# Kernel optimization log

Measured on AMD Instinct MI355X. Metric: run time of the kernel, lower is better.

The kernel has to match this reference:

```python
import jax, jax.numpy as jnp
import numpy as np

B, T, N = 16, 1024, 512        # batch, time tokens, neurons
DK_T, DK_S = 64, 128           # key dims (temporal, spatial)
# dim_T = N, dim_S = T, dim_value_T = N (required by cross einsum), heads = 1


def setup_inputs() -> dict:
    key = jax.random.key(0)
    ks = jax.random.split(key, 11)
    return {
        "x_T": jax.random.normal(ks[0], (B, T, N), jnp.float32),
        "x_S": jax.random.normal(ks[1], (B, N, T), jnp.float32),
        "Wq_T": jax.random.normal(ks[2], (N, DK_T), jnp.float32) * 0.05,
        "Wk_T": jax.random.normal(ks[3], (N, DK_T), jnp.float32) * 0.05,
        "Wv_T": jax.random.normal(ks[4], (N, N), jnp.float32) * 0.05,
        "Wq_S": jax.random.normal(ks[5], (T, DK_S), jnp.float32) * 0.05,
        "Wk_S": jax.random.normal(ks[6], (T, DK_S), jnp.float32) * 0.05,
        "Wout_T": jax.random.normal(ks[7], (N, N), jnp.float32) * 0.05,
        "bout_T": jax.random.normal(ks[8], (N,), jnp.float32) * 0.05,
        "bias_T": jax.random.normal(ks[9], (1, 1, 1, DK_T), jnp.float32),
        "bias_S": jax.random.normal(ks[10], (1, 1, 1, DK_S), jnp.float32),
    }


def reference(x_T, x_S, Wq_T, Wk_T, Wv_T, Wq_S, Wk_S, Wout_T, bout_T, bias_T, bias_S):
    scale_T = DK_T ** -0.5
    scale_S = DK_S ** -0.5
    # Temporal attention: tokens along time axis, heads=1 -> add h axis
    q_T = (x_T @ Wq_T)[:, None] * scale_T          # [b,1,t,dk_T]
    k_T = (x_T @ Wk_T)[:, None]                    # [b,1,t,dk_T]
    v_T = (x_T @ Wv_T)[:, None]                    # [b,1,t,n]  (dim_value_T = n)
    logits_T = jnp.einsum('bhid,bhjd->bhij', q_T + bias_T, k_T)  # [b,1,t,t]
    attn_T = jax.nn.softmax(logits_T, axis=-1)
    out_T = jnp.einsum('bhij,bhjd->bhid', attn_T, v_T)            # [b,1,t,n]
    # Spatial attention: tokens along neuron axis
    q_S = (x_S @ Wq_S)[:, None] * scale_S          # [b,1,n,dk_S]
    k_S = (x_S @ Wk_S)[:, None]                    # [b,1,n,dk_S]
    logits_S = jnp.einsum('bhid,bhjd->bhij', q_S + bias_S, k_S)   # [b,1,n,n]
    attn_S = jax.nn.softmax(logits_S, axis=-1)
    # spatial_temporal_1 cross combination: attn_S mixes the neuron axis of out_T
    out_T = jnp.einsum('bhij,bhtj->bhti', attn_S, out_T)          # [b,1,t,n]
    out_T = out_T.reshape(B, T, N)                 # 'b h t d -> b t (h d)'
    out_T = out_T @ Wout_T + bout_T                # to_out_T
    return jnp.transpose(out_T, (0, 2, 1))         # [b, n, t]
```

## Files before the change

### kernel.cpp

```cpp
#include <hip/hip_runtime.h>
#include <cstddef>

typedef short short8 __attribute__((ext_vector_type(8)));
typedef unsigned short ushortx8 __attribute__((ext_vector_type(8)));
typedef float floatx4 __attribute__((ext_vector_type(4)));

__device__ __forceinline__ unsigned int bf16_rne(float x) {
    unsigned int u = __float_as_uint(x);
    return (u + 0x7fffu + ((u >> 16) & 1u)) >> 16;
}

__device__ __forceinline__ void split4(const floatx4 v,
                                       unsigned long long& hp,
                                       unsigned long long& lp) {
    unsigned int h[4], l[4];
    #pragma unroll
    for (int j = 0; j < 4; ++j) {
        h[j] = bf16_rne(v[j]);
        float hf = __uint_as_float(h[j] << 16);
        l[j] = bf16_rne(v[j] - hf);
    }
    hp = (unsigned long long)(h[0] | (h[1] << 16)) |
         ((unsigned long long)(h[2] | (h[3] << 16)) << 32);
    lp = (unsigned long long)(l[0] | (l[1] << 16)) |
         ((unsigned long long)(l[2] | (l[3] << 16)) << 32);
}

__device__ __forceinline__ unsigned long long pack_hi4(const floatx4 v) {
    unsigned int h0 = bf16_rne(v[0]), h1 = bf16_rne(v[1]);
    unsigned int h2 = bf16_rne(v[2]), h3 = bf16_rne(v[3]);
    return (unsigned long long)(h0 | (h1 << 16)) |
           ((unsigned long long)(h2 | (h3 << 16)) << 32);
}

template<int BM, int BN, int AMODE, int BMODE, int OUTMODE, bool HASBIAS>
__global__ __launch_bounds__(256, 2)
void gemm_nt(const void* __restrict__ Ah_, const void* __restrict__ Al_,
             const void* __restrict__ Bh_, const void* __restrict__ Bl_,
             void* __restrict__ C_, void* __restrict__ Cl_,
             const float* __restrict__ bias,
             int K, int lda, int ldb, int ldc,
             long sA, long sB, long sC, float alpha, int nsplit)
{
    constexpr bool ALO = (AMODE == 1 || AMODE == 3);
    constexpr bool BLO = (BMODE == 1 || BMODE == 3);
    constexpr int LS = 40;
    __shared__ unsigned short Ash[2][BM][LS];
    __shared__ unsigned short Als[2][ALO ? BM : 1][LS];
    __shared__ unsigned short Bsh[2][BN][LS];
    __shared__ unsigned short Bls[2][BLO ? BN : 1][LS];

    const unsigned int gx = gridDim.x;
    const unsigned int nwg = gx * gridDim.y;
    unsigned int flat = blockIdx.y * gx + blockIdx.x;
    {
        unsigned int qq = nwg >> 3, rr = nwg & 7;
        unsigned int xcd = flat & 7, idx = flat >> 3;
        flat = (xcd < rr) ? (xcd * (qq + 1) + idx)
                          : (rr * (qq + 1) + (xcd - rr) * qq + idx);
    }
    const int b   = blockIdx.z;
    const int bm0 = (flat / gx) * BM;
    const int bn0 = (flat % gx) * BN;
    const int tid  = threadIdx.x;
    const int lane = tid & 63;
    const int wid  = tid >> 6;
    const int wr = wid >> 1, wc = wid & 1;
    constexpr int WM = BM / 2, WN = BN / 2;
    constexpr int FM = WM / 16, FN = WN / 16;
    floatx4 acc[FM][FN] = {};
    const int l15  = lane & 15;
    const int koff = (lane >> 4) * 8;

    constexpr int ACHF = BM * 32 / 4, NAF0 = (ACHF + 255) / 256;
    constexpr int ACHH = BM * 32 / 8, NAH0 = (ACHH + 255) / 256;
    constexpr int BCHF = BN * 32 / 4, NBF0 = (BCHF + 255) / 256;
    constexpr int BCHH = BN * 32 / 8, NBH0 = (BCHH + 255) / 256;
    constexpr int NAF = (AMODE <= 1) ? NAF0 : 1;
    constexpr int NAH = (AMODE >= 2) ? NAH0 : 1;
    constexpr int NBF = (BMODE <= 1) ? NBF0 : 1;
    constexpr int NBH = (BMODE >= 2) ? NBH0 : 1;
    floatx4  aF[NAF], bF[NBF];
    ushortx8 aH[NAH], aL[NAH], bH[NBH], bL[NBH];

    auto loadA = [&](int k0) {
        if (AMODE <= 1) {
            const float* A = (const float*)Ah_ + (long)b * sA;
            #pragma unroll
            for (int i = 0; i < NAF; ++i) {
                int idx = i * 256 + tid;
                if (ACHF % 256 == 0 || idx < ACHF) {
                    int flatc = idx * 4;
                    int r = flatc >> 5, c = flatc & 31;
                    aF[i] = *(const floatx4*)(A + (long)(bm0 + r) * lda + k0 + c);
                }
            }
        } else {
            const unsigned short* A  = (const unsigned short*)Ah_ + (long)b * sA;
            const unsigned short* Al = (const unsigned short*)Al_ + (long)b * sA;
            #pragma unroll
            for (int i = 0; i < NAH; ++i) {
                int idx = i * 256 + tid;
                if (ACHH % 256 == 0 || idx < ACHH) {
                    int flatc = idx * 8;
                    int r = flatc >> 5, c = flatc & 31;
                    aH[i] = *(const ushortx8*)(A + (long)(bm0 + r) * lda + k0 + c);
                    if (AMODE == 3)
                        aL[i] = *(const ushortx8*)(Al + (long)(bm0 + r) * lda + k0 + c);
                }
            }
        }
    };
    auto loadB = [&](int k0) {
        if (BMODE <= 1) {
            const float* Bp = (const float*)Bh_ + (long)b * sB;
            #pragma unroll
            for (int i = 0; i < NBF; ++i) {
                int idx = i * 256 + tid;
                if (BCHF % 256 == 0 || idx < BCHF) {
                    int flatc = idx * 4;
                    int r = flatc >> 5, c = flatc & 31;
                    bF[i] = *(const floatx4*)(Bp + (long)(bn0 + r) * ldb + k0 + c);
                }
            }
        } else {
            const unsigned short* Bp = (const unsigned short*)Bh_ + (long)b * sB;
            const unsigned short* Bl = (const unsigned short*)Bl_ + (long)b * sB;
            #pragma unroll
            for (int i = 0; i < NBH; ++i) {
                int idx = i * 256 + tid;
                if (BCHH % 256 == 0 || idx < BCHH) {
                    int flatc = idx * 8;
                    int r = flatc >> 5, c = flatc & 31;
                    bH[i] = *(const ushortx8*)(Bp + (long)(bn0 + r) * ldb + k0 + c);
                    if (BMODE == 3)
                        bL[i] = *(const ushortx8*)(Bl + (long)(bn0 + r) * ldb + k0 + c);
                }
            }
        }
    };
    auto writeA = [&](int bf) {
        if (AMODE <= 1) {
            #pragma unroll
            for (int i = 0; i < NAF; ++i) {
                int idx = i * 256 + tid;
                if (ACHF % 256 == 0 || idx < ACHF) {
                    int flatc = idx * 4;
                    int r = flatc >> 5, c = flatc & 31;
                    if (AMODE == 1) {
                        unsigned long long hp, lp; split4(aF[i], hp, lp);
                        *(unsigned long long*)&Ash[bf][r][c] = hp;
                        *(unsigned long long*)&Als[bf][r][c] = lp;
                    } else {
                        *(unsigned long long*)&Ash[bf][r][c] = pack_hi4(aF[i]);
                    }
                }
            }
        } else {
            #pragma unroll
            for (int i = 0; i < NAH; ++i) {
                int idx = i * 256 + tid;
                if (ACHH % 256 == 0 || idx < ACHH) {
                    int flatc = idx * 8;
                    int r = flatc >> 5, c = flatc & 31;
                    *(ushortx8*)&Ash[bf][r][c] = aH[i];
                    if (AMODE == 3) *(ushortx8*)&Als[bf][r][c] = aL[i];
                }
            }
        }
    };
    auto writeB = [&](int bf) {
        if (BMODE <= 1) {
            #pragma unroll
            for (int i = 0; i < NBF; ++i) {
                int idx = i * 256 + tid;
                if (BCHF % 256 == 0 || idx < BCHF) {
                    int flatc = idx * 4;
                    int r = flatc >> 5, c = flatc & 31;
                    if (BMODE == 1) {
                        unsigned long long hp, lp; split4(bF[i], hp, lp);
                        *(unsigned long long*)&Bsh[bf][r][c] = hp;
                        *(unsigned long long*)&Bls[bf][r][c] = lp;
                    } else {
                        *(unsigned long long*)&Bsh[bf][r][c] = pack_hi4(bF[i]);
                    }
                }
            }
        } else {
            #pragma unroll
            for (int i = 0; i < NBH; ++i) {
                int idx = i * 256 + tid;
                if (BCHH % 256 == 0 || idx < BCHH) {
                    int flatc = idx * 8;
                    int r = flatc >> 5, c = flatc & 31;
                    *(ushortx8*)&Bsh[bf][r][c] = bH[i];
                    if (BMODE == 3) *(ushortx8*)&Bls[bf][r][c] = bL[i];
                }
            }
        }
    };
    auto compute = [&](int bf) {
        short8 ah[FM], al[FM], bh[FN], bl[FN];
        #pragma unroll
        for (int mi = 0; mi < FM; ++mi) {
            ah[mi] = *(const short8*)&Ash[bf][wr * WM + mi * 16 + l15][koff];
            if (ALO) al[mi] = *(const short8*)&Als[bf][wr * WM + mi * 16 + l15][koff];
        }
        #pragma unroll
        for (int ni = 0; ni < FN; ++ni) {
            bh[ni] = *(const short8*)&Bsh[bf][wc * WN + ni * 16 + l15][koff];
            if (BLO) bl[ni] = *(const short8*)&Bls[bf][wc * WN + ni * 16 + l15][koff];
        }
        #pragma unroll
        for (int mi = 0; mi < FM; ++mi)
            #pragma unroll
            for (int ni = 0; ni < FN; ++ni) {
                if (ALO)
                    acc[mi][ni] = __builtin_amdgcn_mfma_f32_16x16x32_bf16(
                        al[mi], bh[ni], acc[mi][ni], 0, 0, 0);
                if (BLO)
                    acc[mi][ni] = __builtin_amdgcn_mfma_f32_16x16x32_bf16(
                        ah[mi], bl[ni], acc[mi][ni], 0, 0, 0);
                acc[mi][ni] = __builtin_amdgcn_mfma_f32_16x16x32_bf16(
                    ah[mi], bh[ni], acc[mi][ni], 0, 0, 0);
            }
    };

    loadA(0); loadB(0);
    writeA(0); writeB(0);
    __syncthreads();
    int cur = 0;
    for (int k0 = 32; k0 < K; k0 += 32) {
        loadA(k0); loadB(k0);
        compute(cur);
        writeA(cur ^ 1); writeB(cur ^ 1);
        __syncthreads();
        cur ^= 1;
    }
    compute(cur);

    const int rq = (lane >> 4) * 4;
    #pragma unroll
    for (int mi = 0; mi < FM; ++mi) {
        #pragma unroll
        for (int ni = 0; ni < FN; ++ni) {
            int gm = bm0 + wr * WM + mi * 16 + rq;
            int gn = bn0 + wc * WN + ni * 16 + l15;
            float ae = (gn < nsplit) ? alpha : 1.0f;
            float be = 0.f;
            if (HASBIAS) be = (gn < nsplit) ? bias[gn] : 0.0f;
            float vals[4];
            #pragma unroll
            for (int j = 0; j < 4; ++j) vals[j] = acc[mi][ni][j] * ae + be;
            if (OUTMODE == 0) {
                float* C = (float*)C_ + (long)b * sC;
                #pragma unroll
                for (int j = 0; j < 4; ++j) C[(long)(gm + j) * ldc + gn] = vals[j];
            } else if (OUTMODE == 1) {
                float* C = (float*)C_ + (long)b * sC;
                floatx4 o;
                #pragma unroll
                for (int j = 0; j < 4; ++j) o[j] = vals[j];
                *(floatx4*)(C + (long)gn * ldc + gm) = o;
            } else if (OUTMODE == 2) {
                unsigned short* Ch = (unsigned short*)C_ + (long)b * sC;
                unsigned short* Cl = (unsigned short*)Cl_ + (long)b * sC;
                #pragma unroll
                for (int j = 0; j < 4; ++j) {
                    unsigned int h = bf16_rne(vals[j]);
                    float hf = __uint_as_float(h << 16);
                    unsigned int lo = bf16_rne(vals[j] - hf);
                    Ch[(long)(gm + j) * ldc + gn] = (unsigned short)h;
                    Cl[(long)(gm + j) * ldc + gn] = (unsigned short)lo;
                }
            } else {
                unsigned short* Ch = (unsigned short*)C_ + (long)b * sC;
                #pragma unroll
                for (int j = 0; j < 4; ++j)
                    Ch[(long)(gm + j) * ldc + gn] = (unsigned short)bf16_rne(vals[j]);
            }
        }
    }
}

template<int COLS, int DK, int LDQK>
__global__ __launch_bounds__(256, 2)
void qk_softmax(const unsigned short* __restrict__ qk_h,
                const unsigned short* __restrict__ qk_l,
                unsigned short* __restrict__ P)
{
    constexpr int WCOLS = COLS / 4;
    constexpr int FN = WCOLS / 16;
    constexpr int QPAD = DK + 24;
    __shared__ unsigned short Qh[32][QPAD];
    __shared__ unsigned short Ql[32][QPAD];
    __shared__ float red[32][4];
    __shared__ unsigned short Pl[32][COLS + 8];

    const int b  = blockIdx.y;
    const int q0 = blockIdx.x * 32;
    const long rowBase = (long)b * COLS;
    const int tid = threadIdx.x;
    const int lane = tid & 63, wid = tid >> 6;
    const int l15 = lane & 15, g = lane >> 4;
    const int koff = g * 8;

    constexpr int QCH = DK / 8;
    for (int i = tid; i < 32 * QCH; i += 256) {
        int r = i / QCH, c = (i % QCH) * 8;
        *(ushortx8*)&Qh[r][c] = *(const ushortx8*)(qk_h + (rowBase + q0 + r) * LDQK + c);
        *(ushortx8*)&Ql[r][c] = *(const ushortx8*)(qk_l + (rowBase + q0 + r) * LDQK + c);
    }
    __syncthreads();

    floatx4 acc[2][FN] = {};
    const unsigned short* kh = qk_h + rowBase * LDQK + DK;
    const unsigned short* kl = qk_l + rowBase * LDQK + DK;

    #pragma unroll
    for (int kk = 0; kk < DK; kk += 32) {
        short8 ah[2], al[2];
        #pragma unroll
        for (int mi = 0; mi < 2; ++mi) {
            ah[mi] = *(const short8*)&Qh[mi * 16 + l15][kk + koff];
            al[mi] = *(const short8*)&Ql[mi * 16 + l15][kk + koff];
        }
        #pragma unroll
        for (int ni = 0; ni < FN; ++ni) {
            long krow = wid * WCOLS + ni * 16 + l15;
            short8 bh = *(const short8*)(kh + krow * LDQK + kk + koff);
            short8 bl = *(const short8*)(kl + krow * LDQK + kk + koff);
            #pragma unroll
            for (int mi = 0; mi < 2; ++mi) {
                acc[mi][ni] = __builtin_amdgcn_mfma_f32_16x16x32_bf16(al[mi], bh, acc[mi][ni], 0, 0, 0);
                acc[mi][ni] = __builtin_amdgcn_mfma_f32_16x16x32_bf16(ah[mi], bl, acc[mi][ni], 0, 0, 0);
                acc[mi][ni] = __builtin_amdgcn_mfma_f32_16x16x32_bf16(ah[mi], bh, acc[mi][ni], 0, 0, 0);
            }
        }
    }

    float pm[2][4];
    #pragma unroll
    for (int mi = 0; mi < 2; ++mi)
        #pragma unroll
        for (int j = 0; j < 4; ++j) {
            float m = acc[mi][0][j];
            #pragma unroll
            for (int ni = 1; ni < FN; ++ni) m = fmaxf(m, acc[mi][ni][j]);
            pm[mi][j] = m;
        }
    #pragma unroll
    for (int msk = 1; msk < 16; msk <<= 1) {
        #pragma unroll
        for (int mi = 0; mi < 2; ++mi)
            #pragma unroll
            for (int j = 0; j < 4; ++j)
                pm[mi][j] = fmaxf(pm[mi][j], __shfl_xor(pm[mi][j], msk));
    }
    if (l15 == 0) {
        #pragma unroll
        for (int mi = 0; mi < 2; ++mi)
            #pragma unroll
            for (int j = 0; j < 4; ++j) red[mi * 16 + g * 4 + j][wid] = pm[mi][j];
    }
    __syncthreads();
    float rm[2][4];
    #pragma unroll
    for (int mi = 0; mi < 2; ++mi)
        #pragma unroll
        for (int j = 0; j < 4; ++j) {
            const float* r4 = red[mi * 16 + g * 4 + j];
            rm[mi][j] = fmaxf(fmaxf(r4[0], r4[1]), fmaxf(r4[2], r4[3]));
        }
    __syncthreads();

    float ps[2][4] = {};
    #pragma unroll
    for (int mi = 0; mi < 2; ++mi)
        #pragma unroll
        for (int ni = 0; ni < FN; ++ni)
            #pragma unroll
            for (int j = 0; j < 4; ++j) {
                float e = __expf(acc[mi][ni][j] - rm[mi][j]);
                acc[mi][ni][j] = e;
                ps[mi][j] += e;
            }
    #pragma unroll
    for (int msk = 1; msk < 16; msk <<= 1) {
        #pragma unroll
        for (int mi = 0; mi < 2; ++mi)
            #pragma unroll
            for (int j = 0; j < 4; ++j)
                ps[mi][j] += __shfl_xor(ps[mi][j], msk);
    }
    if (l15 == 0) {
        #pragma unroll
        for (int mi = 0; mi < 2; ++mi)
            #pragma unroll
            for (int j = 0; j < 4; ++j) red[mi * 16 + g * 4 + j][wid] = ps[mi][j];
    }
    __syncthreads();
    float inv[2][4];
    #pragma unroll
    for (int mi = 0; mi < 2; ++mi)
        #pragma unroll
        for (int j = 0; j < 4; ++j) {
            const float* r4 = red[mi * 16 + g * 4 + j];
            inv[mi][j] = 1.0f / (r4[0] + r4[1] + r4[2] + r4[3]);
        }

    #pragma unroll
    for (int mi = 0; mi < 2; ++mi)
        #pragma unroll
        for (int ni = 0; ni < FN; ++ni)
            #pragma unroll
            for (int j = 0; j < 4; ++j)
                Pl[mi * 16 + g * 4 + j][wid * WCOLS + ni * 16 + l15] =
                    (unsigned short)bf16_rne(acc[mi][ni][j] * inv[mi][j]);
    __syncthreads();

    constexpr int PCH = COLS / 8;
    for (int i = tid; i < 32 * PCH; i += 256) {
        int r = i / PCH, c = (i % PCH) * 8;
        *(ushortx8*)(P + (rowBase + q0 + r) * COLS + c) = *(const ushortx8*)&Pl[r][c];
    }
}

__global__ __launch_bounds__(256)
void transpose_split(const float* __restrict__ in,
                     unsigned short* __restrict__ outH,
                     unsigned short* __restrict__ outL,
                     int R, int C, int rowOff, int ldo)
{
    __shared__ float tile[32][33];
    const int tc = blockIdx.x * 32, tr = blockIdx.y * 32;
    const int x = threadIdx.x, y = threadIdx.y;
    #pragma unroll
    for (int i = 0; i < 32; i += 8)
        tile[y + i][x] = in[(long)(tr + y + i) * C + tc + x];
    __syncthreads();
    #pragma unroll
    for (int i = 0; i < 32; i += 8) {
        float v = tile[x][y + i];
        unsigned int h = bf16_rne(v);
        float hf = __uint_as_float(h << 16);
        unsigned int lo = bf16_rne(v - hf);
        long idx = (long)(tc + y + i + rowOff) * ldo + tr + x;
        outH[idx] = (unsigned short)h;
        outL[idx] = (unsigned short)lo;
    }
}

extern "C" void kernel_launch(void* const* d_in, const int* in_sizes, int n_in,
                              void* d_out, int out_size, void* d_ws, size_t ws_size,
                              hipStream_t stream)
{
    (void)in_sizes; (void)n_in; (void)out_size; (void)ws_size;
    const float* x_T    = (const float*)d_in[0];
    const float* x_S    = (const float*)d_in[1];
    const float* Wq_T   = (const float*)d_in[2];
    const float* Wk_T   = (const float*)d_in[3];
    const float* Wv_T   = (const float*)d_in[4];
    const float* Wq_S   = (const float*)d_in[5];
    const float* Wk_S   = (const float*)d_in[6];
    const float* Wout_T = (const float*)d_in[7];
    const float* bout_T = (const float*)d_in[8];
    const float* bias_T = (const float*)d_in[9];
    const float* bias_S = (const float*)d_in[10];
    float* out = (float*)d_out;

    constexpr int B = 16, T = 1024, N = 512, DKT = 64, DKS = 128;
    typedef unsigned short us;

    char* w = (char*)d_ws;
    size_t off = 0;
    auto alloc = [&](size_t bytes) { char* p = w + off; off = (off + bytes + 255) & ~(size_t)255; return p; };
    us* wqkT_h = (us*)alloc(128 * 512 * 2);
    us* wqkT_l = (us*)alloc(128 * 512 * 2);
    us* wvt_h  = (us*)alloc(512 * 512 * 2);
    us* wvt_l  = (us*)alloc(512 * 512 * 2);
    us* wqks_h = (us*)alloc(256 * 1024 * 2);
    us* wqks_l = (us*)alloc(256 * 1024 * 2);
    us* wout_h = (us*)alloc(512 * 512 * 2);
    us* wout_l = (us*)alloc(512 * 512 * 2);
    us* qk_h   = (us*)alloc((size_t)16384 * 128 * 2);
    us* qk_l   = (us*)alloc((size_t)16384 * 128 * 2);
    us* P_T    = (us*)alloc((size_t)B * T * T * 2);
    us* P_S    = (us*)alloc((size_t)B * N * N * 2);
    us* vT_h   = (us*)alloc((size_t)B * N * T * 2);
    us* vT_l   = (us*)alloc((size_t)B * N * T * 2);
    us* outT_h = (us*)alloc((size_t)B * T * N * 2);
    us* outT_l = (us*)alloc((size_t)B * T * N * 2);
    us* out2_h = vT_h;
    us* out2_l = vT_l;

    const float scale_T = 0.125f;
    const float scale_S = 0.088388347648318447f;
    const int BIG = 1 << 30;

    dim3 tb(32, 8);
    transpose_split<<<dim3(2, 16),  tb, 0, stream>>>(Wq_T,   wqkT_h, wqkT_l, 512, 64,   0, 512);
    transpose_split<<<dim3(2, 16),  tb, 0, stream>>>(Wk_T,   wqkT_h, wqkT_l, 512, 64,  64, 512);
    transpose_split<<<dim3(16, 16), tb, 0, stream>>>(Wv_T,   wvt_h,  wvt_l,  512, 512,  0, 512);
    transpose_split<<<dim3(4, 32),  tb, 0, stream>>>(Wq_S,   wqks_h, wqks_l, 1024, 128, 0, 1024);
    transpose_split<<<dim3(4, 32),  tb, 0, stream>>>(Wk_S,   wqks_h, wqks_l, 1024, 128, 128, 1024);
    transpose_split<<<dim3(16, 16), tb, 0, stream>>>(Wout_T, wout_h, wout_l, 512, 512,  0, 512);

    gemm_nt<32, 128, 1, 3, 2, true><<<dim3(1, 512, 1), 256, 0, stream>>>(
        x_T, nullptr, wqkT_h, wqkT_l, qk_h, qk_l, bias_T,
        512, 512, 512, 128, 0, 0, 0, scale_T, 64);
    gemm_nt<128, 128, 3, 0, 3, false><<<dim3(8, 4, B), 256, 0, stream>>>(
        wvt_h, wvt_l, x_T, nullptr, vT_h, nullptr, nullptr,
        512, 512, 512, 1024, 0, (long)T * N, (long)N * T, 1.0f, 0);
    qk_softmax<1024, 64, 128><<<dim3(32, 16), 256, 0, stream>>>(qk_h, qk_l, P_T);
    gemm_nt<128, 128, 2, 2, 2, false><<<dim3(4, 8, B), 256, 0, stream>>>(
        P_T, nullptr, vT_h, nullptr, outT_h, outT_l, nullptr,
        1024, 1024, 1024, 512, (long)T * T, (long)N * T, (long)T * N, 1.0f, 0);

    gemm_nt<32, 128, 1, 3, 2, true><<<dim3(2, 256, 1), 256, 0, stream>>>(
        x_S, nullptr, wqks_h, wqks_l, qk_h, qk_l, bias_S,
        1024, 1024, 1024, 256, 0, 0, 0, scale_S, 128);
    qk_softmax<512, 128, 256><<<dim3(16, 16), 256, 0, stream>>>(qk_h, qk_l, P_S);
    gemm_nt<128, 128, 3, 2, 2, false><<<dim3(4, 8, B), 256, 0, stream>>>(
        outT_h, outT_l, P_S, nullptr, out2_h, out2_l, nullptr,
        512, 512, 512, 512, (long)T * N, (long)N * N, (long)T * N, 1.0f, 0);
    gemm_nt<128, 128, 3, 2, 1, true><<<dim3(4, 8, B), 256, 0, stream>>>(
        out2_h, out2_l, wout_h, nullptr, out, nullptr, bout_T,
        512, 512, 512, 1024, (long)T * N, 0, (long)N * T, 1.0f, BIG);
}
```

Before: 221.8 us.

## Split-K the Q/K projection GEMMs with a separate reduce-and-split kernel

Replaces the two Q/K projection GEMMs (x_T and x_S against stacked Wq/Wk) with a dedicated 4-way split-K kernel that writes fp32 partials into the P_T scratch buffer. A reduce kernel then sums the partials, applies scale and bias to the query half, and splits the result into bf16 hi/lo. This raises the block count for these narrow-N projections to improve CU occupancy. In exchange it adds an extra launch and fp32 partial traffic through global memory. It also drops the B-lo product term, which the original mode 2 also lacked.

After: 224.9 us. Within noise of the previous version (+1.4%).

```diff
diff --git a/kernel.cpp b/kernel.cpp
--- a/kernel.cpp
+++ b/kernel.cpp
@@ -3,6 +3,7 @@
 
 typedef short short8 __attribute__((ext_vector_type(8)));
 typedef unsigned short ushortx8 __attribute__((ext_vector_type(8)));
+typedef unsigned short ushortx4 __attribute__((ext_vector_type(4)));
 typedef float floatx4 __attribute__((ext_vector_type(4)));
 
 __device__ __forceinline__ unsigned int bf16_rne(float x) {
@@ -90,8 +91,7 @@
             for (int i = 0; i < NAF; ++i) {
                 int idx = i * 256 + tid;
                 if (ACHF % 256 == 0 || idx < ACHF) {
-                    int flatc = idx * 4;
-                    int r = flatc >> 5, c = flatc & 31;
+                    int fc = idx * 4; int r = fc >> 5, c = fc & 31;
                     aF[i] = *(const floatx4*)(A + (long)(bm0 + r) * lda + k0 + c);
                 }
             }
@@ -102,8 +102,7 @@
             for (int i = 0; i < NAH; ++i) {
                 int idx = i * 256 + tid;
                 if (ACHH % 256 == 0 || idx < ACHH) {
-                    int flatc = idx * 8;
-                    int r = flatc >> 5, c = flatc & 31;
+                    int fc = idx * 8; int r = fc >> 5, c = fc & 31;
                     aH[i] = *(const ushortx8*)(A + (long)(bm0 + r) * lda + k0 + c);
                     if (AMODE == 3)
                         aL[i] = *(const ushortx8*)(Al + (long)(bm0 + r) * lda + k0 + c);
@@ -118,8 +117,7 @@
             for (int i = 0; i < NBF; ++i) {
                 int idx = i * 256 + tid;
                 if (BCHF % 256 == 0 || idx < BCHF) {
-                    int flatc = idx * 4;
-                    int r = flatc >> 5, c = flatc & 31;
+                    int fc = idx * 4; int r = fc >> 5, c = fc & 31;
                     bF[i] = *(const floatx4*)(Bp + (long)(bn0 + r) * ldb + k0 + c);
                 }
             }
@@ -130,8 +128,7 @@
             for (int i = 0; i < NBH; ++i) {
                 int idx = i * 256 + tid;
                 if (BCHH % 256 == 0 || idx < BCHH) {
-                    int flatc = idx * 8;
-                    int r = flatc >> 5, c = flatc & 31;
+                    int fc = idx * 8; int r = fc >> 5, c = fc & 31;
                     bH[i] = *(const ushortx8*)(Bp + (long)(bn0 + r) * ldb + k0 + c);
                     if (BMODE == 3)
                         bL[i] = *(const ushortx8*)(Bl + (long)(bn0 + r) * ldb + k0 + c);
@@ -145,8 +142,7 @@
             for (int i = 0; i < NAF; ++i) {
                 int idx = i * 256 + tid;
                 if (ACHF % 256 == 0 || idx < ACHF) {
-                    int flatc = idx * 4;
-                    int r = flatc >> 5, c = flatc & 31;
+                    int fc = idx * 4; int r = fc >> 5, c = fc & 31;
                     if (AMODE == 1) {
                         unsigned long long hp, lp; split4(aF[i], hp, lp);
                         *(unsigned long long*)&Ash[bf][r][c] = hp;
@@ -161,8 +157,7 @@
             for (int i = 0; i < NAH; ++i) {
                 int idx = i * 256 + tid;
                 if (ACHH % 256 == 0 || idx < ACHH) {
-                    int flatc = idx * 8;
-                    int r = flatc >> 5, c = flatc & 31;
+                    int fc = idx * 8; int r = fc >> 5, c = fc & 31;
                     *(ushortx8*)&Ash[bf][r][c] = aH[i];
                     if (AMODE == 3) *(ushortx8*)&Als[bf][r][c] = aL[i];
                 }
@@ -175,8 +170,7 @@
             for (int i = 0; i < NBF; ++i) {
                 int idx = i * 256 + tid;
                 if (BCHF % 256 == 0 || idx < BCHF) {
-                    int flatc = idx * 4;
-                    int r = flatc >> 5, c = flatc & 31;
+                    int fc = idx * 4; int r = fc >> 5, c = fc & 31;
                     if (BMODE == 1) {
                         unsigned long long hp, lp; split4(bF[i], hp, lp);
                         *(unsigned long long*)&Bsh[bf][r][c] = hp;
@@ -191,8 +185,7 @@
             for (int i = 0; i < NBH; ++i) {
                 int idx = i * 256 + tid;
                 if (BCHH % 256 == 0 || idx < BCHH) {
-                    int flatc = idx * 8;
-                    int r = flatc >> 5, c = flatc & 31;
+                    int fc = idx * 8; int r = fc >> 5, c = fc & 31;
                     *(ushortx8*)&Bsh[bf][r][c] = bH[i];
                     if (BMODE == 3) *(ushortx8*)&Bls[bf][r][c] = bL[i];
                 }
@@ -283,6 +276,114 @@
     }
 }
 
+template<int KCH>
+__global__ __launch_bounds__(256, 6)
+void proj_splitk(const float* __restrict__ A, const unsigned short* __restrict__ Bp,
+                 float* __restrict__ Cpart, int lda, int ldb, int ldc, long MN)
+{
+    __shared__ unsigned short Ah[32][40];
+    __shared__ unsigned short Al[32][40];
+    __shared__ unsigned short Bs[128][40];
+
+    const int tid = threadIdx.x;
+    const int lane = tid & 63, wid = tid >> 6;
+    const int wr = wid >> 1, wc = wid & 1;
+    const int l15 = lane & 15, g = lane >> 4;
+    const int koff = g * 8;
+    const int bm0 = blockIdx.y * 32;
+    const int bn0 = blockIdx.x * 128;
+    const int kbase = blockIdx.z * KCH;
+
+    const int ar = tid >> 3, ac = (tid & 7) * 4;
+    floatx4 aReg;
+    ushortx8 bReg[2];
+
+    auto load = [&](int k0) {
+        aReg = *(const floatx4*)(A + (long)(bm0 + ar) * lda + k0 + ac);
+        #pragma unroll
+        for (int i = 0; i < 2; ++i) {
+            int fc = (i * 256 + tid) * 8;
+            int r = fc >> 5, c = fc & 31;
+            bReg[i] = *(const ushortx8*)(Bp + (long)(bn0 + r) * ldb + k0 + c);
+        }
+    };
+    auto store_lds = [&]() {
+        unsigned long long hp, lp; split4(aReg, hp, lp);
+        *(unsigned long long*)&Ah[ar][ac] = hp;
+        *(unsigned long long*)&Al[ar][ac] = lp;
+        #pragma unroll
+        for (int i = 0; i < 2; ++i) {
+            int fc = (i * 256 + tid) * 8;
+            int r = fc >> 5, c = fc & 31;
+            *(ushortx8*)&Bs[r][c] = bReg[i];
+        }
+    };
+
+    floatx4 acc[4] = {};
+    auto compute = [&]() {
+        short8 ah = *(const short8*)&Ah[wr * 16 + l15][koff];
+        short8 al = *(const short8*)&Al[wr * 16 + l15][koff];
+        #pragma unroll
+        for (int ni = 0; ni < 4; ++ni) {
+            short8 bh = *(const short8*)&Bs[wc * 64 + ni * 16 + l15][koff];
+            acc[ni] = __builtin_amdgcn_mfma_f32_16x16x32_bf16(al, bh, acc[ni], 0, 0, 0);
+            acc[ni] = __builtin_amdgcn_mfma_f32_16x16x32_bf16(ah, bh, acc[ni], 0, 0, 0);
+        }
+    };
+
+    load(kbase);
+    store_lds();
+    __syncthreads();
+    #pragma unroll 1
+    for (int s = 1; s < KCH / 32; ++s) {
+        load(kbase + s * 32);
+        compute();
+        __syncthreads();
+        store_lds();
+        __syncthreads();
+    }
+    compute();
+
+    float* C = Cpart + (long)blockIdx.z * MN;
+    #pragma unroll
+    for (int ni = 0; ni < 4; ++ni) {
+        int gn = bn0 + wc * 64 + ni * 16 + l15;
+        #pragma unroll
+        for (int j = 0; j < 4; ++j)
+            C[(long)(bm0 + wr * 16 + g * 4 + j) * ldc + gn] = acc[ni][j];
+    }
+}
+
+__global__ __launch_bounds__(256)
+void reduce_split(const float* __restrict__ Cp, long MN, int colMask, int nsplit,
+                  float alpha, const float* __restrict__ bias,
+                  unsigned short* __restrict__ H, unsigned short* __restrict__ L)
+{
+    long n4 = MN >> 2;
+    for (long i = (long)blockIdx.x * 256 + threadIdx.x; i < n4;
+         i += (long)gridDim.x * 256) {
+        long e = i << 2;
+        floatx4 v = *(const floatx4*)(Cp + e);
+        v += *(const floatx4*)(Cp + MN + e);
+        v += *(const floatx4*)(Cp + 2 * MN + e);
+        v += *(const floatx4*)(Cp + 3 * MN + e);
+        int colb = (int)(e & colMask);
+        ushortx4 h4, l4;
+        #pragma unroll
+        for (int j = 0; j < 4; ++j) {
+            float x = v[j];
+            int col = colb + j;
+            if (col < nsplit) x = x * alpha + bias[col];
+            unsigned int h = bf16_rne(x);
+            float hf = __uint_as_float(h << 16);
+            h4[j] = (unsigned short)h;
+            l4[j] = (unsigned short)bf16_rne(x - hf);
+        }
+        *(ushortx4*)(H + e) = h4;
+        *(ushortx4*)(L + e) = l4;
+    }
+}
+
 template<int COLS, int DK, int LDQK>
 __global__ __launch_bounds__(256, 2)
 void qk_softmax(const unsigned short* __restrict__ qk_h,
@@ -493,6 +594,7 @@
     us* outT_l = (us*)alloc((size_t)B * T * N * 2);
     us* out2_h = vT_h;
     us* out2_l = vT_l;
+    float* partial = (float*)P_T;
 
     const float scale_T = 0.125f;
     const float scale_S = 0.088388347648318447f;
@@ -506,9 +608,10 @@
     transpose_split<<<dim3(4, 32),  tb, 0, stream>>>(Wk_S,   wqks_h, wqks_l, 1024, 128, 128, 1024);
     transpose_split<<<dim3(16, 16), tb, 0, stream>>>(Wout_T, wout_h, wout_l, 512, 512,  0, 512);
 
-    gemm_nt<32, 128, 1, 3, 2, true><<<dim3(1, 512, 1), 256, 0, stream>>>(
-        x_T, nullptr, wqkT_h, wqkT_l, qk_h, qk_l, bias_T,
-        512, 512, 512, 128, 0, 0, 0, scale_T, 64);
+    proj_splitk<128><<<dim3(1, 512, 4), 256, 0, stream>>>(
+        x_T, wqkT_h, partial, 512, 512, 128, (long)16384 * 128);
+    reduce_split<<<1024, 256, 0, stream>>>(
+        partial, (long)16384 * 128, 127, 64, scale_T, bias_T, qk_h, qk_l);
     gemm_nt<128, 128, 3, 0, 3, false><<<dim3(8, 4, B), 256, 0, stream>>>(
         wvt_h, wvt_l, x_T, nullptr, vT_h, nullptr, nullptr,
         512, 512, 512, 1024, 0, (long)T * N, (long)N * T, 1.0f, 0);
@@ -517,9 +620,10 @@
         P_T, nullptr, vT_h, nullptr, outT_h, outT_l, nullptr,
         1024, 1024, 1024, 512, (long)T * T, (long)N * T, (long)T * N, 1.0f, 0);
 
-    gemm_nt<32, 128, 1, 3, 2, true><<<dim3(2, 256, 1), 256, 0, stream>>>(
-        x_S, nullptr, wqks_h, wqks_l, qk_h, qk_l, bias_S,
-        1024, 1024, 1024, 256, 0, 0, 0, scale_S, 128);
+    proj_splitk<256><<<dim3(2, 256, 4), 256, 0, stream>>>(
+        x_S, wqks_h, partial, 1024, 1024, 256, (long)8192 * 256);
+    reduce_split<<<1024, 256, 0, stream>>>(
+        partial, (long)8192 * 256, 255, 128, scale_S, bias_S, qk_h, qk_l);
     qk_softmax<512, 128, 256><<<dim3(16, 16), 256, 0, stream>>>(qk_h, qk_l, P_S);
     gemm_nt<128, 128, 3, 2, 2, false><<<dim3(4, 8, B), 256, 0, stream>>>(
         outT_h, outT_l, P_S, nullptr, out2_h, out2_l, nullptr,
```
